# Optimization experiments

Measured on AMD Instinct MI355X. Metric: run time of the kernel, lower is better.

Reference implementation:

```python
import jax, jax.numpy as jnp
import numpy as np

NUM_CLASSES = 80
STRIDES = (8, 16, 32)
INPUT_SIZE = 640
DIST_THRESH_SQ = 64.0 * 64.0  # assignment uses euclidean dist < 64; compare squared


def make_anchors(input_size):
    pts = []
    for s in STRIDES:
        n = input_size // s
        yv, xv = np.meshgrid(np.arange(n), np.arange(n), indexing='ij')
        g = np.stack([xv, yv], -1).reshape(-1, 2).astype(np.float32) * s + s // 2
        pts.append(g)
    return jnp.asarray(np.concatenate(pts, 0))  # [A, 2]


def bce_logits(x, t):
    # BCEWithLogits, elementwise: -(t*log_sigmoid(x) + (1-t)*log_sigmoid(-x))
    return -(t * jax.nn.log_sigmoid(x) + (1.0 - t) * jax.nn.log_sigmoid(-x))


def iou_loss(pred_boxes, target_boxes):
    # pred: (cx, cy, log_w, log_h); target: (cx, cy, w, h) in pixels
    pc = pred_boxes[:, :2]
    ps = jnp.exp(pred_boxes[:, 2:4])
    p1 = pc - ps / 2.0
    p2 = pc + ps / 2.0
    t1 = target_boxes[:, :2] - target_boxes[:, 2:4] / 2.0
    t2 = target_boxes[:, :2] + target_boxes[:, 2:4] / 2.0
    i1 = jnp.maximum(p1, t1)
    i2 = jnp.minimum(p2, t2)
    inter = jnp.clip(i2[:, 0] - i1[:, 0], 0.0) * jnp.clip(i2[:, 1] - i1[:, 1], 0.0)
    pa = (p2[:, 0] - p1[:, 0]) * (p2[:, 1] - p1[:, 1])
    ta = (t2[:, 0] - t1[:, 0]) * (t2[:, 1] - t1[:, 1])
    union = pa + ta - inter
    return 1.0 - inter / (union + 1e-06)


def setup_inputs() -> dict:
    key = jax.random.key(0)
    k1, k2, k3, k4, k5 = jax.random.split(key, 5)
    B, M = 64, 50
    A = sum((INPUT_SIZE // s) ** 2 for s in STRIDES)  # 8400
    predictions = jax.random.normal(k1, (B, A, 5 + NUM_CLASSES), dtype=jnp.float32)
    cls = jax.random.randint(k2, (B, M), 0, NUM_CLASSES).astype(jnp.float32)
    valid = jax.random.uniform(k3, (B, M)) < 0.6
    cls = jnp.where(valid, cls, -1.0)
    centers = jax.random.uniform(k4, (B, M, 2), minval=0.05, maxval=0.95)
    wh = jax.random.uniform(k5, (B, M, 2), minval=0.02, maxval=0.3)
    targets = jnp.concatenate([cls[..., None], centers, wh], axis=-1).astype(jnp.float32)
    return {"predictions": predictions, "targets": targets, "input_size": 640}


def _per_image(pred, tgt, anchors, num_classes, input_size):
    # pred: [A, 5+C], tgt: [M, 5]
    valid = tgt[:, 0] >= 0.0                              # [M]
    gt_cls = tgt[:, 0].astype(jnp.int32)                  # [M]
    gt_boxes = tgt[:, 1:5] * input_size                   # [M, 4] pixels
    diff = gt_boxes[:, None, :2] - anchors[None, :, :]    # [M, A, 2]
    d2 = jnp.sum(diff * diff, axis=-1)                    # [M, A] squared dist
    d2 = jnp.where(valid[:, None], d2, jnp.inf)
    matched = jnp.argmin(d2, axis=0)                      # [A]
    min_d2 = jnp.min(d2, axis=0)                          # [A]
    pos = min_d2 < DIST_THRESH_SQ                         # [A]
    posf = pos.astype(pred.dtype)
    num_pos = posf.sum()

    obj_loss = bce_logits(pred[:, 4], posf).mean()

    cls_t = jax.nn.one_hot(gt_cls[matched], num_classes, dtype=pred.dtype)  # [A, C]
    cls_bce = bce_logits(pred[:, 5:], cls_t)                                # [A, C]
    denom = jnp.maximum(num_pos, 1.0)
    cls_loss = jnp.where(num_pos > 0,
                         (cls_bce * posf[:, None]).sum() / (denom * num_classes), 0.0)

    iou_l = iou_loss(pred[:, :4], gt_boxes[matched])      # [A]
    box_loss = jnp.where(num_pos > 0, (iou_l * posf).sum() / denom, 0.0)
    return obj_loss, cls_loss, box_loss, num_pos


def reference(predictions, targets, input_size):
    anchors = make_anchors(int(input_size))               # [A, 2]
    fsize = jnp.float32(input_size)
    obj, cls, box, npos = jax.vmap(
        lambda p, t: _per_image(p, t, anchors, NUM_CLASSES, fsize)
    )(predictions, targets)
    obj_loss = obj.sum()
    cls_loss = cls.sum()
    box_loss = box.sum()
    num_fg = npos.sum()
    total = 5.0 * box_loss + obj_loss + cls_loss
    return total, box_loss, obj_loss, cls_loss, num_fg
```

## Files before the change

### kernel.cpp

```cpp
#include <hip/hip_runtime.h>
#include <math.h>

#define NUM_CLASSES 80
#define MT 50
#define ATOT 8400
#define CH 85
#define BLOCK 256
#define CHUNK 256
#define NBY 33

__device__ __forceinline__ float softplus_fast(float x) {
    return fmaxf(x, 0.0f) + __logf(1.0f + __expf(-fabsf(x)));
}

__global__ __launch_bounds__(BLOCK) void yolox_fused(
        const float* __restrict__ pred,
        const float* __restrict__ tgt,
        const int*   __restrict__ isz,
        float* __restrict__ acc) {
    const int b  = blockIdx.y;
    const int by = blockIdx.x;
    const int a0 = by * CHUNK;
    const int nanch = min(CHUNK, ATOT - a0);

    __shared__ float2 sxy[64];
    __shared__ float2 swh[64];
    __shared__ float  scls[64];
    __shared__ int    snv;
    __shared__ float  sposf[CHUNK];

    if (threadIdx.x < 64) {
        const int m = threadIdx.x;
        const float fsize = (float)(*isz);
        float c = -1.0f, x = 0.f, y = 0.f, w = 0.f, h = 0.f;
        if (m < MT) {
            const float* tb = tgt + (size_t)b * MT * 5 + (size_t)m * 5;
            c = tb[0];
            x = tb[1] * fsize; y = tb[2] * fsize;
            w = tb[3] * fsize; h = tb[4] * fsize;
        }
        const bool valid = (m < MT) && (c >= 0.0f);
        const unsigned long long ballot = __ballot(valid);
        const int slot = __popcll(ballot & ((1ull << threadIdx.x) - 1ull));
        if (valid) {
            sxy[slot]  = make_float2(x, y);
            swh[slot]  = make_float2(w, h);
            scls[slot] = c;
        }
        if (m == 0) snv = (int)__popcll(ballot);
    }
    sposf[threadIdx.x] = 0.0f;
    __syncthreads();
    const int nv = snv;

    float box_s = 0.f, np_s = 0.f, cls_s = 0.f, obj_s = 0.f;

    const int a = a0 + threadIdx.x;
    if (threadIdx.x < nanch) {
        float ax, ay;
        if (a < 6400)      { const int yy = a / 80;              const int xx = a - yy * 80;  ax = (float)(xx * 8  + 4);  ay = (float)(yy * 8  + 4); }
        else if (a < 8000) { const int i2 = a - 6400; const int yy = i2 / 40; const int xx = i2 - yy * 40; ax = (float)(xx * 16 + 8);  ay = (float)(yy * 16 + 8); }
        else               { const int i2 = a - 8000; const int yy = i2 / 20; const int xx = i2 - yy * 20; ax = (float)(xx * 32 + 16); ay = (float)(yy * 32 + 16); }

        float best = INFINITY;
        int bestm = 0;
        for (int m = 0; m < nv; ++m) {
            const float2 g = sxy[m];
            const float dx = g.x - ax, dy = g.y - ay;
            const float d2 = dx * dx + dy * dy;
            if (d2 < best) { best = d2; bestm = m; }
        }
        const bool pos = best < 4096.0f;

        if (pos) {
            sposf[threadIdx.x] = 1.0f;
            np_s = 1.0f;
            const float* p = pred + ((size_t)b * ATOT + (size_t)a) * CH;
            const int gcls = (int)scls[bestm];
            cls_s = -p[5 + gcls];

            const float pcx = p[0], pcy = p[1];
            const float pw = __expf(p[2]), ph = __expf(p[3]);
            const float2 g  = sxy[bestm];
            const float2 wh = swh[bestm];
            const float p1x = pcx - pw * 0.5f, p2x = pcx + pw * 0.5f;
            const float p1y = pcy - ph * 0.5f, p2y = pcy + ph * 0.5f;
            const float t1x = g.x - wh.x * 0.5f, t2x = g.x + wh.x * 0.5f;
            const float t1y = g.y - wh.y * 0.5f, t2y = g.y + wh.y * 0.5f;
            const float iw = fminf(p2x, t2x) - fmaxf(p1x, t1x);
            const float ih = fminf(p2y, t2y) - fmaxf(p1y, t1y);
            const float inter = fmaxf(iw, 0.f) * fmaxf(ih, 0.f);
            const float pa = (p2x - p1x) * (p2y - p1y);
            const float ta = (t2x - t1x) * (t2y - t1y);
            const float uni = pa + ta - inter;
            box_s = 1.0f - inter / (uni + 1e-6f);
        }
    }
    __syncthreads();

    const float* base = pred + ((size_t)b * ATOT + (size_t)a0) * CH;
    const int ngroups = (nanch * CH) >> 2;

    #pragma unroll 4
    for (int g = threadIdx.x; g < ngroups; g += BLOCK) {
        const int le0 = g << 2;
        const unsigned la = __umulhi((unsigned)le0, 3233857729u) >> 6;
        const int c0 = le0 - (int)la * CH;
        const float posf = sposf[la];
        const bool mpos = posf > 0.0f;
        const bool need = (c0 >= 1 && c0 <= 4) || (mpos && c0 >= 2);
        if (need) {
            const float4 x4 = *(const float4*)(base + le0);
            const float xs[4] = {x4.x, x4.y, x4.z, x4.w};
            #pragma unroll
            for (int j = 0; j < 4; ++j) {
                const int c = c0 + j;
                if (c == 4) {
                    obj_s += softplus_fast(xs[j]) - posf * xs[j];
                } else if (c >= 5 && c < CH && mpos) {
                    cls_s += softplus_fast(xs[j]);
                }
            }
        }
    }

    float v0 = obj_s, v1 = cls_s, v2 = box_s, v3 = np_s;
    for (int off = 32; off > 0; off >>= 1) {
        v0 += __shfl_down(v0, off, 64);
        v1 += __shfl_down(v1, off, 64);
        v2 += __shfl_down(v2, off, 64);
        v3 += __shfl_down(v3, off, 64);
    }
    __shared__ float sred[BLOCK / 64][4];
    const int wave = threadIdx.x >> 6;
    const int lane = threadIdx.x & 63;
    if (lane == 0) {
        sred[wave][0] = v0; sred[wave][1] = v1;
        sred[wave][2] = v2; sred[wave][3] = v3;
    }
    __syncthreads();
    if (threadIdx.x == 0) {
        float t0 = 0.f, t1 = 0.f, t2 = 0.f, t3 = 0.f;
        #pragma unroll
        for (int w = 0; w < BLOCK / 64; ++w) {
            t0 += sred[w][0]; t1 += sred[w][1];
            t2 += sred[w][2]; t3 += sred[w][3];
        }
        float* slot = acc + ((size_t)b * NBY + by) * 4;
        slot[0] = t0; slot[1] = t1; slot[2] = t2; slot[3] = t3;
    }
}

__global__ __launch_bounds__(BLOCK) void yolox_stage2(
        const float* __restrict__ acc,
        float* __restrict__ out, int B) {
    float obj = 0.f, cls = 0.f, box = 0.f, np = 0.f;
    for (int bb = threadIdx.x; bb < B; bb += BLOCK) {
        float os = 0.f, cs = 0.f, bs = 0.f, ps = 0.f;
        const float* s = acc + (size_t)bb * NBY * 4;
        #pragma unroll
        for (int j = 0; j < NBY; ++j) {
            os += s[j * 4 + 0];
            cs += s[j * 4 + 1];
            bs += s[j * 4 + 2];
            ps += s[j * 4 + 3];
        }
        obj += os * (1.0f / (float)ATOT);
        const float denom = fmaxf(ps, 1.0f);
        cls += (ps > 0.f) ? cs / (denom * (float)NUM_CLASSES) : 0.f;
        box += (ps > 0.f) ? bs / denom : 0.f;
        np  += ps;
    }
    float v0 = obj, v1 = cls, v2 = box, v3 = np;
    for (int off = 32; off > 0; off >>= 1) {
        v0 += __shfl_down(v0, off, 64);
        v1 += __shfl_down(v1, off, 64);
        v2 += __shfl_down(v2, off, 64);
        v3 += __shfl_down(v3, off, 64);
    }
    __shared__ float sred[BLOCK / 64][4];
    const int wave = threadIdx.x >> 6;
    const int lane = threadIdx.x & 63;
    if (lane == 0) {
        sred[wave][0] = v0; sred[wave][1] = v1;
        sred[wave][2] = v2; sred[wave][3] = v3;
    }
    __syncthreads();
    if (threadIdx.x == 0) {
        float t0 = 0.f, t1 = 0.f, t2 = 0.f, t3 = 0.f;
        #pragma unroll
        for (int w = 0; w < BLOCK / 64; ++w) {
            t0 += sred[w][0]; t1 += sred[w][1];
            t2 += sred[w][2]; t3 += sred[w][3];
        }
        out[0] = 5.0f * t2 + t0 + t1;
        out[1] = t2;
        out[2] = t0;
        out[3] = t1;
        out[4] = t3;
    }
}

extern "C" void kernel_launch(void* const* d_in, const int* in_sizes, int n_in,
                              void* d_out, int out_size, void* d_ws, size_t ws_size,
                              hipStream_t stream) {
    const float* pred = (const float*)d_in[0];
    const float* tgt  = (const float*)d_in[1];
    const int*   isz  = (const int*)d_in[2];
    float* out = (float*)d_out;
    float* acc = (float*)d_ws;

    const int B = in_sizes[1] / (MT * 5);

    dim3 grid(NBY, B);
    yolox_fused<<<grid, BLOCK, 0, stream>>>(pred, tgt, isz, acc);
    yolox_stage2<<<1, BLOCK, 0, stream>>>(acc, out, B);
}
```

Before: 276.8 us.

## Split matching and bulk BCE streaming into separate kernels with batched loads

```diff
diff --git a/kernel.cpp b/kernel.cpp
--- a/kernel.cpp
+++ b/kernel.cpp
@@ -5,19 +5,24 @@
 #define MT 50
 #define ATOT 8400
 #define CH 85
+#define EPI (ATOT * CH)
+#define EPG (EPI / 4)
 #define BLOCK 256
 #define CHUNK 256
 #define NBY 33
+#define NX 88
+#define G 8
 
 __device__ __forceinline__ float softplus_fast(float x) {
     return fmaxf(x, 0.0f) + __logf(1.0f + __expf(-fabsf(x)));
 }
 
-__global__ __launch_bounds__(BLOCK) void yolox_fused(
+__global__ __launch_bounds__(BLOCK) void yolox_match(
         const float* __restrict__ pred,
         const float* __restrict__ tgt,
         const int*   __restrict__ isz,
-        float* __restrict__ acc) {
+        int*   __restrict__ gmask,
+        float* __restrict__ accM) {
     const int b  = blockIdx.y;
     const int by = blockIdx.x;
     const int a0 = by * CHUNK;
@@ -27,7 +32,6 @@
     __shared__ float2 swh[64];
     __shared__ float  scls[64];
     __shared__ int    snv;
-    __shared__ float  sposf[CHUNK];
 
     if (threadIdx.x < 64) {
         const int m = threadIdx.x;
@@ -49,11 +53,10 @@
         }
         if (m == 0) snv = (int)__popcll(ballot);
     }
-    sposf[threadIdx.x] = 0.0f;
     __syncthreads();
     const int nv = snv;
 
-    float box_s = 0.f, np_s = 0.f, cls_s = 0.f, obj_s = 0.f;
+    float box_s = 0.f, np_s = 0.f;
 
     const int a = a0 + threadIdx.x;
     if (threadIdx.x < nanch) {
@@ -72,13 +75,11 @@
         }
         const bool pos = best < 4096.0f;
 
+        gmask[(size_t)b * ATOT + a] = pos ? (int)scls[bestm] : -1;
+
         if (pos) {
-            sposf[threadIdx.x] = 1.0f;
             np_s = 1.0f;
             const float* p = pred + ((size_t)b * ATOT + (size_t)a) * CH;
-            const int gcls = (int)scls[bestm];
-            cls_s = -p[5 + gcls];
-
             const float pcx = p[0], pcy = p[1];
             const float pw = __expf(p[2]), ph = __expf(p[3]);
             const float2 g  = sxy[bestm];
@@ -96,75 +97,112 @@
             box_s = 1.0f - inter / (uni + 1e-6f);
         }
     }
-    __syncthreads();
-
-    const float* base = pred + ((size_t)b * ATOT + (size_t)a0) * CH;
-    const int ngroups = (nanch * CH) >> 2;
-
-    #pragma unroll 4
-    for (int g = threadIdx.x; g < ngroups; g += BLOCK) {
-        const int le0 = g << 2;
-        const unsigned la = __umulhi((unsigned)le0, 3233857729u) >> 6;
-        const int c0 = le0 - (int)la * CH;
-        const float posf = sposf[la];
-        const bool mpos = posf > 0.0f;
-        const bool need = (c0 >= 1 && c0 <= 4) || (mpos && c0 >= 2);
-        if (need) {
-            const float4 x4 = *(const float4*)(base + le0);
-            const float xs[4] = {x4.x, x4.y, x4.z, x4.w};
-            #pragma unroll
-            for (int j = 0; j < 4; ++j) {
-                const int c = c0 + j;
-                if (c == 4) {
-                    obj_s += softplus_fast(xs[j]) - posf * xs[j];
-                } else if (c >= 5 && c < CH && mpos) {
-                    cls_s += softplus_fast(xs[j]);
-                }
+
+    float v2 = box_s, v3 = np_s;
+    for (int off = 32; off > 0; off >>= 1) {
+        v2 += __shfl_down(v2, off, 64);
+        v3 += __shfl_down(v3, off, 64);
+    }
+    __shared__ float sred[BLOCK / 64][2];
+    const int wave = threadIdx.x >> 6;
+    const int lane = threadIdx.x & 63;
+    if (lane == 0) { sred[wave][0] = v2; sred[wave][1] = v3; }
+    __syncthreads();
+    if (threadIdx.x == 0) {
+        float t2 = 0.f, t3 = 0.f;
+        #pragma unroll
+        for (int w = 0; w < BLOCK / 64; ++w) { t2 += sred[w][0]; t3 += sred[w][1]; }
+        float* slot = accM + ((size_t)b * NBY + by) * 2;
+        slot[0] = t2; slot[1] = t3;
+    }
+}
+
+__global__ __launch_bounds__(BLOCK) void yolox_bulk(
+        const float* __restrict__ pred,
+        const int*   __restrict__ gmask,
+        float* __restrict__ accB) {
+    const int b   = blockIdx.y;
+    const int tid = threadIdx.x;
+    const int base_g = blockIdx.x * (BLOCK * G);
+
+    const float* pbase = pred + (size_t)b * EPI;
+    const int*   mbase = gmask + (size_t)b * ATOT;
+
+    int  mk[G], c0k[G], lek[G];
+    bool need[G];
+
+    #pragma unroll
+    for (int k = 0; k < G; ++k) {
+        const int g  = base_g + k * BLOCK + tid;
+        const bool ok = g < EPG;
+        const int le = g << 2;
+        const unsigned la = __umulhi((unsigned)le, 3233857729u) >> 6;
+        lek[k] = le;
+        c0k[k] = le - (int)la * CH;
+        mk[k]  = ok ? mbase[la] : -1;
+        need[k] = ok && ((c0k[k] >= 1 && c0k[k] <= 4) || (mk[k] >= 0 && c0k[k] >= 2));
+    }
+
+    float4 x[G];
+    #pragma unroll
+    for (int k = 0; k < G; ++k) {
+        x[k] = need[k] ? *(const float4*)(pbase + lek[k])
+                       : make_float4(0.f, 0.f, 0.f, 0.f);
+    }
+
+    float obj_s = 0.f, cls_s = 0.f;
+    #pragma unroll
+    for (int k = 0; k < G; ++k) {
+        if (!need[k]) continue;
+        const int c0 = c0k[k];
+        const int m  = mk[k];
+        const bool mpos = m >= 0;
+        const float xs[4] = {x[k].x, x[k].y, x[k].z, x[k].w};
+        #pragma unroll
+        for (int j = 0; j < 4; ++j) {
+            const int c = c0 + j;
+            const float xv = xs[j];
+            if (c == 4) {
+                obj_s += softplus_fast(xv) - (mpos ? xv : 0.0f);
+            } else if (c >= 5 && c < CH && mpos) {
+                cls_s += softplus_fast(xv) - ((c - 5 == m) ? xv : 0.0f);
             }
         }
     }
 
-    float v0 = obj_s, v1 = cls_s, v2 = box_s, v3 = np_s;
+    float v0 = obj_s, v1 = cls_s;
     for (int off = 32; off > 0; off >>= 1) {
         v0 += __shfl_down(v0, off, 64);
         v1 += __shfl_down(v1, off, 64);
-        v2 += __shfl_down(v2, off, 64);
-        v3 += __shfl_down(v3, off, 64);
-    }
-    __shared__ float sred[BLOCK / 64][4];
+    }
+    __shared__ float sred[BLOCK / 64][2];
     const int wave = threadIdx.x >> 6;
     const int lane = threadIdx.x & 63;
-    if (lane == 0) {
-        sred[wave][0] = v0; sred[wave][1] = v1;
-        sred[wave][2] = v2; sred[wave][3] = v3;
-    }
+    if (lane == 0) { sred[wave][0] = v0; sred[wave][1] = v1; }
     __syncthreads();
     if (threadIdx.x == 0) {
-        float t0 = 0.f, t1 = 0.f, t2 = 0.f, t3 = 0.f;
-        #pragma unroll
-        for (int w = 0; w < BLOCK / 64; ++w) {
-            t0 += sred[w][0]; t1 += sred[w][1];
-            t2 += sred[w][2]; t3 += sred[w][3];
-        }
-        float* slot = acc + ((size_t)b * NBY + by) * 4;
-        slot[0] = t0; slot[1] = t1; slot[2] = t2; slot[3] = t3;
+        float t0 = 0.f, t1 = 0.f;
+        #pragma unroll
+        for (int w = 0; w < BLOCK / 64; ++w) { t0 += sred[w][0]; t1 += sred[w][1]; }
+        float* slot = accB + ((size_t)b * NX + blockIdx.x) * 2;
+        slot[0] = t0; slot[1] = t1;
     }
 }
 
 __global__ __launch_bounds__(BLOCK) void yolox_stage2(
-        const float* __restrict__ acc,
+        const float* __restrict__ accM,
+        const float* __restrict__ accB,
         float* __restrict__ out, int B) {
     float obj = 0.f, cls = 0.f, box = 0.f, np = 0.f;
     for (int bb = threadIdx.x; bb < B; bb += BLOCK) {
-        float os = 0.f, cs = 0.f, bs = 0.f, ps = 0.f;
-        const float* s = acc + (size_t)bb * NBY * 4;
-        #pragma unroll
-        for (int j = 0; j < NBY; ++j) {
-            os += s[j * 4 + 0];
-            cs += s[j * 4 + 1];
-            bs += s[j * 4 + 2];
-            ps += s[j * 4 + 3];
-        }
+        float bs = 0.f, ps = 0.f;
+        const float* sM = accM + (size_t)bb * NBY * 2;
+        #pragma unroll
+        for (int j = 0; j < NBY; ++j) { bs += sM[j * 2 + 0]; ps += sM[j * 2 + 1]; }
+        float os = 0.f, cs = 0.f;
+        const float* sB = accB + (size_t)bb * NX * 2;
+        #pragma unroll 8
+        for (int j = 0; j < NX; ++j) { os += sB[j * 2 + 0]; cs += sB[j * 2 + 1]; }
         obj += os * (1.0f / (float)ATOT);
         const float denom = fmaxf(ps, 1.0f);
         cls += (ps > 0.f) ? cs / (denom * (float)NUM_CLASSES) : 0.f;
@@ -208,11 +246,18 @@
     const float* tgt  = (const float*)d_in[1];
     const int*   isz  = (const int*)d_in[2];
     float* out = (float*)d_out;
-    float* acc = (float*)d_ws;
 
     const int B = in_sizes[1] / (MT * 5);
 
-    dim3 grid(NBY, B);
-    yolox_fused<<<grid, BLOCK, 0, stream>>>(pred, tgt, isz, acc);
-    yolox_stage2<<<1, BLOCK, 0, stream>>>(acc, out, B);
-}
+    int*   gmask = (int*)d_ws;
+    float* accM  = (float*)((char*)d_ws + (size_t)B * ATOT * sizeof(int));
+    float* accB  = accM + (size_t)B * NBY * 2;
+
+    dim3 gridM(NBY, B);
+    yolox_match<<<gridM, BLOCK, 0, stream>>>(pred, tgt, isz, gmask, accM);
+
+    dim3 gridB(NX, B);
+    yolox_bulk<<<gridB, BLOCK, 0, stream>>>(pred, gmask, accB);
+
+    yolox_stage2<<<1, BLOCK, 0, stream>>>(accM, accB, out, B);
+}
```

Result: faster. 269.8 us (-2.5%).

## Use 80-anchor tiles with unconditional batched float4 loads and shared-memory box gather

Applied to the files above, without the earlier changes.

```diff
diff --git a/kernel.cpp b/kernel.cpp
--- a/kernel.cpp
+++ b/kernel.cpp
@@ -6,8 +6,11 @@
 #define ATOT 8400
 #define CH 85
 #define BLOCK 256
-#define CHUNK 256
-#define NBY 33
+#define TILE 80
+#define NBLK 105
+#define EPB (TILE * CH)
+#define GPB (EPB / 4)
+#define NITER 7
 
 __device__ __forceinline__ float softplus_fast(float x) {
     return fmaxf(x, 0.0f) + __logf(1.0f + __expf(-fabsf(x)));
@@ -18,19 +21,22 @@
         const float* __restrict__ tgt,
         const int*   __restrict__ isz,
         float* __restrict__ acc) {
-    const int b  = blockIdx.y;
-    const int by = blockIdx.x;
-    const int a0 = by * CHUNK;
-    const int nanch = min(CHUNK, ATOT - a0);
+    const int b   = blockIdx.y;
+    const int blk = blockIdx.x;
+    const int a0  = blk * TILE;
+    const int tid = threadIdx.x;
 
     __shared__ float2 sxy[64];
     __shared__ float2 swh[64];
     __shared__ float  scls[64];
     __shared__ int    snv;
-    __shared__ float  sposf[CHUNK];
-
-    if (threadIdx.x < 64) {
-        const int m = threadIdx.x;
+    __shared__ float  sposf[TILE];
+    __shared__ int    sgcls[TILE];
+    __shared__ int    sbestm[TILE];
+    __shared__ float  sbox[TILE][4];
+
+    if (tid < 64) {
+        const int m = tid;
         const float fsize = (float)(*isz);
         float c = -1.0f, x = 0.f, y = 0.f, w = 0.f, h = 0.f;
         if (m < MT) {
@@ -41,7 +47,7 @@
         }
         const bool valid = (m < MT) && (c >= 0.0f);
         const unsigned long long ballot = __ballot(valid);
-        const int slot = __popcll(ballot & ((1ull << threadIdx.x) - 1ull));
+        const int slot = __popcll(ballot & ((1ull << tid) - 1ull));
         if (valid) {
             sxy[slot]  = make_float2(x, y);
             swh[slot]  = make_float2(w, h);
@@ -49,14 +55,11 @@
         }
         if (m == 0) snv = (int)__popcll(ballot);
     }
-    sposf[threadIdx.x] = 0.0f;
     __syncthreads();
     const int nv = snv;
 
-    float box_s = 0.f, np_s = 0.f, cls_s = 0.f, obj_s = 0.f;
-
-    const int a = a0 + threadIdx.x;
-    if (threadIdx.x < nanch) {
+    if (tid < TILE) {
+        const int a = a0 + tid;
         float ax, ay;
         if (a < 6400)      { const int yy = a / 80;              const int xx = a - yy * 80;  ax = (float)(xx * 8  + 4);  ay = (float)(yy * 8  + 4); }
         else if (a < 8000) { const int i2 = a - 6400; const int yy = i2 / 40; const int xx = i2 - yy * 40; ax = (float)(xx * 16 + 8);  ay = (float)(yy * 16 + 8); }
@@ -71,57 +74,72 @@
             if (d2 < best) { best = d2; bestm = m; }
         }
         const bool pos = best < 4096.0f;
-
-        if (pos) {
-            sposf[threadIdx.x] = 1.0f;
-            np_s = 1.0f;
-            const float* p = pred + ((size_t)b * ATOT + (size_t)a) * CH;
-            const int gcls = (int)scls[bestm];
-            cls_s = -p[5 + gcls];
-
-            const float pcx = p[0], pcy = p[1];
-            const float pw = __expf(p[2]), ph = __expf(p[3]);
-            const float2 g  = sxy[bestm];
-            const float2 wh = swh[bestm];
-            const float p1x = pcx - pw * 0.5f, p2x = pcx + pw * 0.5f;
-            const float p1y = pcy - ph * 0.5f, p2y = pcy + ph * 0.5f;
-            const float t1x = g.x - wh.x * 0.5f, t2x = g.x + wh.x * 0.5f;
-            const float t1y = g.y - wh.y * 0.5f, t2y = g.y + wh.y * 0.5f;
-            const float iw = fminf(p2x, t2x) - fmaxf(p1x, t1x);
-            const float ih = fminf(p2y, t2y) - fmaxf(p1y, t1y);
-            const float inter = fmaxf(iw, 0.f) * fmaxf(ih, 0.f);
-            const float pa = (p2x - p1x) * (p2y - p1y);
-            const float ta = (t2x - t1x) * (t2y - t1y);
-            const float uni = pa + ta - inter;
-            box_s = 1.0f - inter / (uni + 1e-6f);
-        }
+        sposf[tid]  = pos ? 1.0f : 0.0f;
+        sgcls[tid]  = pos ? (int)scls[bestm] : -1;
+        sbestm[tid] = bestm;
     }
     __syncthreads();
 
     const float* base = pred + ((size_t)b * ATOT + (size_t)a0) * CH;
-    const int ngroups = (nanch * CH) >> 2;
-
-    #pragma unroll 4
-    for (int g = threadIdx.x; g < ngroups; g += BLOCK) {
-        const int le0 = g << 2;
-        const unsigned la = __umulhi((unsigned)le0, 3233857729u) >> 6;
-        const int c0 = le0 - (int)la * CH;
-        const float posf = sposf[la];
-        const bool mpos = posf > 0.0f;
-        const bool need = (c0 >= 1 && c0 <= 4) || (mpos && c0 >= 2);
-        if (need) {
-            const float4 x4 = *(const float4*)(base + le0);
-            const float xs[4] = {x4.x, x4.y, x4.z, x4.w};
-            #pragma unroll
-            for (int j = 0; j < 4; ++j) {
-                const int c = c0 + j;
-                if (c == 4) {
-                    obj_s += softplus_fast(xs[j]) - posf * xs[j];
-                } else if (c >= 5 && c < CH && mpos) {
-                    cls_s += softplus_fast(xs[j]);
-                }
+
+    float4 x[NITER];
+    int    cc[NITER], la[NITER];
+    bool   ok[NITER];
+    #pragma unroll
+    for (int k = 0; k < NITER; ++k) {
+        const int g  = k * BLOCK + tid;
+        ok[k] = (g < GPB);
+        const int le = g << 2;
+        const unsigned u = __umulhi((unsigned)le, 3233857729u) >> 6;
+        la[k] = (int)u;
+        cc[k] = le - (int)u * CH;
+        x[k] = ok[k] ? *(const float4*)(base + le)
+                     : make_float4(0.f, 0.f, 0.f, 0.f);
+    }
+
+    float obj_s = 0.f, cls_s = 0.f;
+    #pragma unroll
+    for (int k = 0; k < NITER; ++k) {
+        if (!ok[k]) continue;
+        const float xs[4] = {x[k].x, x[k].y, x[k].z, x[k].w};
+        #pragma unroll
+        for (int j = 0; j < 4; ++j) {
+            int c  = cc[k] + j;
+            int lj = la[k];
+            if (c >= CH) { c -= CH; ++lj; }
+            const float xv = xs[j];
+            const float pf = sposf[lj];
+            const float sp = softplus_fast(xv);
+            if (c < 4) {
+                sbox[lj][c] = xv;
+            } else if (c == 4) {
+                obj_s += sp - pf * xv;
+            } else {
+                cls_s += pf * (sp - ((c - 5 == sgcls[lj]) ? xv : 0.0f));
             }
         }
+    }
+    __syncthreads();
+
+    float box_s = 0.f, np_s = 0.f;
+    if (tid < TILE && sposf[tid] > 0.0f) {
+        np_s = 1.0f;
+        const float pcx = sbox[tid][0], pcy = sbox[tid][1];
+        const float pw = __expf(sbox[tid][2]), ph = __expf(sbox[tid][3]);
+        const int bestm = sbestm[tid];
+        const float2 g  = sxy[bestm];
+        const float2 wh = swh[bestm];
+        const float p1x = pcx - pw * 0.5f, p2x = pcx + pw * 0.5f;
+        const float p1y = pcy - ph * 0.5f, p2y = pcy + ph * 0.5f;
+        const float t1x = g.x - wh.x * 0.5f, t2x = g.x + wh.x * 0.5f;
+        const float t1y = g.y - wh.y * 0.5f, t2y = g.y + wh.y * 0.5f;
+        const float iw = fminf(p2x, t2x) - fmaxf(p1x, t1x);
+        const float ih = fminf(p2y, t2y) - fmaxf(p1y, t1y);
+        const float inter = fmaxf(iw, 0.f) * fmaxf(ih, 0.f);
+        const float pa = (p2x - p1x) * (p2y - p1y);
+        const float ta = (t2x - t1x) * (t2y - t1y);
+        const float uni = pa + ta - inter;
+        box_s = 1.0f - inter / (uni + 1e-6f);
     }
 
     float v0 = obj_s, v1 = cls_s, v2 = box_s, v3 = np_s;
@@ -132,21 +150,21 @@
         v3 += __shfl_down(v3, off, 64);
     }
     __shared__ float sred[BLOCK / 64][4];
-    const int wave = threadIdx.x >> 6;
-    const int lane = threadIdx.x & 63;
+    const int wave = tid >> 6;
+    const int lane = tid & 63;
     if (lane == 0) {
         sred[wave][0] = v0; sred[wave][1] = v1;
         sred[wave][2] = v2; sred[wave][3] = v3;
     }
     __syncthreads();
-    if (threadIdx.x == 0) {
+    if (tid == 0) {
         float t0 = 0.f, t1 = 0.f, t2 = 0.f, t3 = 0.f;
         #pragma unroll
         for (int w = 0; w < BLOCK / 64; ++w) {
             t0 += sred[w][0]; t1 += sred[w][1];
             t2 += sred[w][2]; t3 += sred[w][3];
         }
-        float* slot = acc + ((size_t)b * NBY + by) * 4;
+        float* slot = acc + ((size_t)b * NBLK + blk) * 4;
         slot[0] = t0; slot[1] = t1; slot[2] = t2; slot[3] = t3;
     }
 }
@@ -157,9 +175,9 @@
     float obj = 0.f, cls = 0.f, box = 0.f, np = 0.f;
     for (int bb = threadIdx.x; bb < B; bb += BLOCK) {
         float os = 0.f, cs = 0.f, bs = 0.f, ps = 0.f;
-        const float* s = acc + (size_t)bb * NBY * 4;
-        #pragma unroll
-        for (int j = 0; j < NBY; ++j) {
+        const float* s = acc + (size_t)bb * NBLK * 4;
+        #pragma unroll 8
+        for (int j = 0; j < NBLK; ++j) {
             os += s[j * 4 + 0];
             cs += s[j * 4 + 1];
             bs += s[j * 4 + 2];
@@ -212,7 +230,7 @@
 
     const int B = in_sizes[1] / (MT * 5);
 
-    dim3 grid(NBY, B);
+    dim3 grid(NBLK, B);
     yolox_fused<<<grid, BLOCK, 0, stream>>>(pred, tgt, isz, acc);
     yolox_stage2<<<1, BLOCK, 0, stream>>>(acc, out, B);
 }
```

After: 274.3 us. No clear change (-0.9%).
